# Kernel tuning notes

Measured on AMD Instinct MI355X. Metric: run time of the kernel, lower is better.

The kernel has to match this reference:

```python
import jax, jax.numpy as jnp
import numpy as np

EMBED_DIM = 1024
NUM_HEADS = 16
HEAD_DIM = EMBED_DIM // NUM_HEADS
B, T = 4, 2048


def setup_inputs() -> dict:
    key = jax.random.key(0)
    ks = jax.random.split(key, 5)
    s = 0.02
    return {
        "x": jax.random.normal(ks[0], (B, T, EMBED_DIM), dtype=jnp.float32),
        "qkv_w": jax.random.normal(ks[1], (3 * EMBED_DIM, EMBED_DIM), dtype=jnp.float32) * s,
        "qkv_b": jax.random.normal(ks[2], (3 * EMBED_DIM,), dtype=jnp.float32) * s,
        "out_w": jax.random.normal(ks[3], (EMBED_DIM, EMBED_DIM), dtype=jnp.float32) * s,
        "out_b": jax.random.normal(ks[4], (EMBED_DIM,), dtype=jnp.float32) * s,
    }


def reference(x, qkv_w, qkv_b, out_w, out_b):
    b, t, c = x.shape
    h, d = NUM_HEADS, HEAD_DIM
    # qkv projection: Linear uses y = x @ W^T + b
    qkv = jnp.einsum("btc,fc->btf", x, qkv_w) + qkv_b  # [B,T,3C]
    q, k, v = jnp.split(qkv, 3, axis=-1)
    # [B, H, T, D]
    q = q.reshape(b, t, h, d).transpose(0, 2, 1, 3)
    k = k.reshape(b, t, h, d).transpose(0, 2, 1, 3)
    v = v.reshape(b, t, h, d).transpose(0, 2, 1, 3)
    scores = jnp.einsum("bhqd,bhkd->bhqk", q, k) / jnp.sqrt(jnp.float32(d))
    causal = jnp.tril(jnp.ones((t, t), dtype=bool))
    scores = jnp.where(causal, scores, -jnp.inf)
    attn = jax.nn.softmax(scores, axis=-1)
    o = jnp.einsum("bhqk,bhkd->bhqd", attn, v)
    o = o.transpose(0, 2, 1, 3).reshape(b, t, c)
    return jnp.einsum("btc,fc->btf", o, out_w) + out_b
```

## Files before the change

### kernel.cpp

```cpp
#include <hip/hip_runtime.h>
#include <hip/hip_bf16.h>
#include <math.h>

#define SEQ   2048
#define NTOK  8192
#define EMB   1024
#define QKVF  3072

typedef __bf16 bf16;
typedef __bf16 bf16x8 __attribute__((ext_vector_type(8)));
typedef __bf16 bf16x4 __attribute__((ext_vector_type(4)));
typedef float  f32x4  __attribute__((ext_vector_type(4)));

__device__ __forceinline__ void gload_lds16(const bf16* g, bf16* l) {
    __builtin_amdgcn_global_load_lds(
        (const __attribute__((address_space(1))) unsigned int*)g,
        (__attribute__((address_space(3))) unsigned int*)l,
        16, 0, 0);
}

__global__ __launch_bounds__(256) void cvt_f32_bf16(const float* __restrict__ in,
                                                    bf16* __restrict__ out, int n) {
    int i = (blockIdx.x * 256 + threadIdx.x) * 4;
    if (i >= n) return;
    float4 f = *reinterpret_cast<const float4*>(in + i);
    bf16x4 o;
    o[0] = (bf16)f.x; o[1] = (bf16)f.y; o[2] = (bf16)f.z; o[3] = (bf16)f.w;
    *reinterpret_cast<bf16x4*>(out + i) = o;
}

template <int NF, bool BF16OUT>
__global__ __launch_bounds__(512, 2) void gemm_bt8(const bf16* __restrict__ A,
                                                   const bf16* __restrict__ Bm,
                                                   const float* __restrict__ bias,
                                                   void* __restrict__ out,
                                                   int M, int N, int K) {
    constexpr int NBR = NF / 2;
    constexpr int WN  = NBR + 2;
    __shared__ bf16 As[2][256 * 64];
    __shared__ bf16 Bs[2][2][NF * 64 * 32];

    const int nbx = N / (NF * 64);
    const int nwg = nbx * (M >> 8);
    const int q8  = nwg >> 3;
    const int swz = ((int)blockIdx.x & 7) * q8 + ((int)blockIdx.x >> 3);
    const int bx  = swz % nbx;
    const int by  = swz / nbx;

    const int tid  = threadIdx.x;
    const int lane = tid & 63;
    const int wid  = tid >> 6;
    const int wr   = wid >> 2, wc = wid & 3;
    const int lr   = lane & 15, hi = lane >> 4;
    const size_t brow = (size_t)by * 256;
    const size_t bcol = (size_t)bx * (NF * 64);

    const f32x4 fzero = {0.f, 0.f, 0.f, 0.f};
    f32x4 acc[8][NF];
#pragma unroll
    for (int m = 0; m < 8; ++m)
#pragma unroll
        for (int n = 0; n < NF; ++n) acc[m][n] = fzero;

#define STAGE_A_ROUND(b, kt, r) do {                                            \
    const int row_ = (r) * 64 + (tid >> 3);                                     \
    const int cg_  = (tid & 7) ^ (row_ & 7);                                    \
    gload_lds16(A + (brow + row_) * (size_t)K + (size_t)(kt) * 64 + cg_ * 8,    \
                &As[b][(r) * 4096 + tid * 8]);                                  \
} while (0)
#define STAGE_B_ROUND(b, kt, kkp, rr) do {                                      \
    const int row_ = (rr) * 128 + (tid >> 2);                                   \
    const int cg_  = (tid & 3) ^ (row_ & 3);                                    \
    gload_lds16(Bm + (bcol + row_) * (size_t)K + (size_t)(kt) * 64 +            \
                    (kkp) * 32 + cg_ * 8,                                       \
                &Bs[b][kkp][(rr) * 4096 + tid * 8]);                            \
} while (0)
#define ISSUE_G1(b, kt) do { STAGE_A_ROUND(b, kt, 0); STAGE_A_ROUND(b, kt, 2);  \
    for (int rr_ = 0; rr_ < NBR; ++rr_) STAGE_B_ROUND(b, kt, 0, rr_); } while (0)
#define ISSUE_G2(b, kt) do {                                                    \
    for (int rr_ = 0; rr_ < NBR; ++rr_) STAGE_B_ROUND(b, kt, 1, rr_); } while (0)
#define ISSUE_G3(b, kt) do { STAGE_A_ROUND(b, kt, 1); STAGE_A_ROUND(b, kt, 3); } while (0)

#define READ_A(b, mh, kk, dst) do {                                             \
    _Pragma("unroll")                                                           \
    for (int i_ = 0; i_ < 4; ++i_) {                                            \
        const int row_ = wr * 128 + (mh) * 64 + i_ * 16 + lr;                   \
        dst[i_] = *reinterpret_cast<const bf16x8*>(                             \
            (const char*)&As[b][0] + row_ * 128 +                               \
            (((kk) * 64 + hi * 16) ^ ((row_ & 7) << 4)));                       \
    }                                                                           \
} while (0)
#define READ_B(b, kk, dst) do {                                                 \
    _Pragma("unroll")                                                           \
    for (int n_ = 0; n_ < NF; ++n_) {                                           \
        const int row_ = wc * (NF * 16) + n_ * 16 + lr;                         \
        dst[n_] = *reinterpret_cast<const bf16x8*>(                             \
            (const char*)&Bs[b][kk][0] + row_ * 64 +                            \
            ((hi * 16) ^ ((row_ & 3) << 4)));                                   \
    }                                                                           \
} while (0)
#define DO_MFMA(mh, afr, bfr) do {                                              \
    __builtin_amdgcn_s_setprio(1);                                              \
    _Pragma("unroll")                                                           \
    for (int i_ = 0; i_ < 4; ++i_)                                              \
        _Pragma("unroll")                                                       \
        for (int n_ = 0; n_ < NF; ++n_)                                         \
            acc[(mh) * 4 + i_][n_] = __builtin_amdgcn_mfma_f32_16x16x32_bf16(   \
                afr[i_], bfr[n_], acc[(mh) * 4 + i_][n_], 0, 0, 0);             \
    __builtin_amdgcn_s_setprio(0);                                              \
} while (0)

    const int NT = K >> 6;

    ISSUE_G1(0, 0);
    ISSUE_G2(0, 0);
    ISSUE_G3(0, 0);
    asm volatile("s_waitcnt vmcnt(%0)" :: "i"(WN) : "memory");
    __builtin_amdgcn_s_barrier();

    bf16x8 af[4], bk0[NF], bk1[NF];

    for (int kt = 0; kt < NT; ++kt) {
        const int  b    = kt & 1;
        const int  nb   = b ^ 1;
        const bool last = (kt == NT - 1);

        if (!last) ISSUE_G1(nb, kt + 1);
        READ_A(b, 0, 0, af);
        READ_B(b, 0, bk0);
        if (last) asm volatile("s_waitcnt vmcnt(0)" ::: "memory");
        else      asm volatile("s_waitcnt vmcnt(%0)" :: "i"(WN) : "memory");
        __builtin_amdgcn_s_barrier();
        DO_MFMA(0, af, bk0);
        __builtin_amdgcn_s_barrier();

        if (!last) ISSUE_G2(nb, kt + 1);
        READ_A(b, 0, 1, af);
        READ_B(b, 1, bk1);
        __builtin_amdgcn_s_barrier();
        DO_MFMA(0, af, bk1);
        __builtin_amdgcn_s_barrier();

        if (!last) ISSUE_G3(nb, kt + 1);
        READ_A(b, 1, 1, af);
        __builtin_amdgcn_s_barrier();
        DO_MFMA(1, af, bk1);
        __builtin_amdgcn_s_barrier();

        READ_A(b, 1, 0, af);
        if (!last) asm volatile("s_waitcnt vmcnt(%0)" :: "i"(WN) : "memory");
        __builtin_amdgcn_s_barrier();
        DO_MFMA(1, af, bk0);
        __builtin_amdgcn_s_barrier();
    }

#pragma unroll
    for (int mf = 0; mf < 8; ++mf)
#pragma unroll
        for (int n = 0; n < NF; ++n)
#pragma unroll
            for (int r = 0; r < 4; ++r) {
                const size_t row = brow + wr * 128 + mf * 16 + hi * 4 + r;
                const size_t col = bcol + wc * (NF * 16) + n * 16 + lr;
                const float v = acc[mf][n][r] + bias[col];
                if (BF16OUT)
                    ((bf16*)out)[row * (size_t)N + col] = (bf16)v;
                else
                    ((float*)out)[row * (size_t)N + col] = v;
            }
#undef STAGE_A_ROUND
#undef STAGE_B_ROUND
#undef ISSUE_G1
#undef ISSUE_G2
#undef ISSUE_G3
#undef READ_A
#undef READ_B
#undef DO_MFMA
}

__global__ __launch_bounds__(256) void attn_kernel(const bf16* __restrict__ qkv,
                                                   bf16* __restrict__ o) {
    const int bid = blockIdx.x;
    const int qt  = 15 - (bid >> 6);
    const int bh  = bid & 63;
    const int h   = bh & 15;
    const int b   = bh >> 4;
    const int qbase = qt * 128;

    const int tid  = threadIdx.x;
    const int wv   = tid >> 6;
    const int lane = tid & 63;
    const int lr   = lane & 15, hi = lane >> 4;

    __shared__ bf16 Ks[64 * 64];
    __shared__ bf16 Vt[64 * 64];
    __shared__ bf16 Pl[4 * 32 * 64];

    char* Ksb = (char*)Ks;
    char* Vtb = (char*)Vt;
    char* Pb  = (char*)(Pl + wv * 2048);

    const size_t tokbase = (size_t)b * SEQ;

    bf16x8 aq[2][2];
#pragma unroll
    for (int qf = 0; qf < 2; ++qf) {
        const bf16* qg = qkv + (tokbase + qbase + wv * 32 + qf * 16 + lr) * (size_t)QKVF
                         + h * 64;
#pragma unroll
        for (int kk = 0; kk < 2; ++kk)
            aq[qf][kk] = *reinterpret_cast<const bf16x8*>(qg + kk * 32 + hi * 8);
    }

    const f32x4 fzero = {0.f, 0.f, 0.f, 0.f};
    f32x4 oacc[2][4];
#pragma unroll
    for (int qf = 0; qf < 2; ++qf)
#pragma unroll
        for (int n = 0; n < 4; ++n) oacc[qf][n] = fzero;
    float m_r[2] = {-__builtin_inff(), -__builtin_inff()};
    float l_r[2] = {0.f, 0.f};

    const int nkv = qt * 2 + 2;
    const float SC = 0.125f * 1.44269504f;

    const int vk0 = tid >> 3;
    const int vc  = tid & 7;

    for (int kt = 0; kt < nkv; ++kt) {
        const size_t kvrow = tokbase + (size_t)kt * 64;
        __syncthreads();

#pragma unroll
        for (int j = 0; j < 2; ++j) {
            const int kr = wv * 16 + j * 8 + (lane >> 3);
            const int cg = (lane & 7) ^ ((lane >> 3) & 7);
            gload_lds16(qkv + (kvrow + kr) * (size_t)QKVF + EMB + h * 64 + cg * 8,
                        &Ks[(wv * 16 + j * 8) * 64 + lane * 8]);
        }

        {
            bf16x8 v0 = *reinterpret_cast<const bf16x8*>(
                qkv + (kvrow + vk0) * (size_t)QKVF + 2 * EMB + h * 64 + vc * 8);
            bf16x8 v1 = *reinterpret_cast<const bf16x8*>(
                qkv + (kvrow + vk0 + 32) * (size_t)QKVF + 2 * EMB + h * 64 + vc * 8);
#pragma unroll
            for (int jj = 0; jj < 8; ++jj) {
                const int d = vc * 8 + jj;
                char* row = Vtb + d * 128;
                *(bf16*)(row + ((vk0 * 2) ^ (vc << 4)))        = v0[jj];
                *(bf16*)(row + (((vk0 + 32) * 2) ^ (vc << 4))) = v1[jj];
            }
        }
        __syncthreads();

        f32x4 s[2][4];
#pragma unroll
        for (int qf = 0; qf < 2; ++qf)
#pragma unroll
            for (int ktile = 0; ktile < 4; ++ktile) s[qf][ktile] = fzero;
#pragma unroll
        for (int ktile = 0; ktile < 4; ++ktile)
#pragma unroll
            for (int kk = 0; kk < 2; ++kk) {
                const int kr = ktile * 16 + lr;
                bf16x8 ak = *reinterpret_cast<const bf16x8*>(
                    Ksb + kr * 128 + ((kk * 64 + hi * 16) ^ ((kr & 7) << 4)));
#pragma unroll
                for (int qf = 0; qf < 2; ++qf)
                    s[qf][ktile] = __builtin_amdgcn_mfma_f32_16x16x32_bf16(
                        ak, aq[qf][kk], s[qf][ktile], 0, 0, 0);
            }

#pragma unroll
        for (int qf = 0; qf < 2; ++qf) {
            const int qglob = qbase + wv * 32 + qf * 16 + lr;
#pragma unroll
            for (int ktile = 0; ktile < 4; ++ktile) {
                const int kg0 = kt * 64 + ktile * 16 + hi * 4;
#pragma unroll
                for (int r = 0; r < 4; ++r) {
                    const float sv = s[qf][ktile][r] * SC;
                    s[qf][ktile][r] = (kg0 + r <= qglob) ? sv : -__builtin_inff();
                }
            }
        }

#pragma unroll
        for (int qf = 0; qf < 2; ++qf) {
            float tm = s[qf][0][0];
#pragma unroll
            for (int ktile = 0; ktile < 4; ++ktile)
#pragma unroll
                for (int r = 0; r < 4; ++r) tm = fmaxf(tm, s[qf][ktile][r]);
            tm = fmaxf(tm, __shfl_xor(tm, 16));
            tm = fmaxf(tm, __shfl_xor(tm, 32));

            const float mn = fmaxf(m_r[qf], tm);
            const float sc = __builtin_amdgcn_exp2f(m_r[qf] - mn);
            m_r[qf] = mn;

            float ts = 0.f;
#pragma unroll
            for (int ktile = 0; ktile < 4; ++ktile)
#pragma unroll
                for (int r = 0; r < 4; ++r) {
                    const float p = __builtin_amdgcn_exp2f(s[qf][ktile][r] - mn);
                    s[qf][ktile][r] = p;
                    ts += p;
                }
            ts += __shfl_xor(ts, 16);
            ts += __shfl_xor(ts, 32);
            l_r[qf] = l_r[qf] * sc + ts;

            float scb[4];
#pragma unroll
            for (int r = 0; r < 4; ++r) scb[r] = __shfl(sc, hi * 4 + r);
#pragma unroll
            for (int n = 0; n < 4; ++n)
#pragma unroll
                for (int r = 0; r < 4; ++r) oacc[qf][n][r] *= scb[r];

            const int q = qf * 16 + lr;
#pragma unroll
            for (int ktile = 0; ktile < 4; ++ktile) {
                bf16x4 p4;
#pragma unroll
                for (int r = 0; r < 4; ++r) p4[r] = (bf16)s[qf][ktile][r];
                *(bf16x4*)(Pb + q * 128 + ((ktile * 32 + hi * 8) ^ ((q & 7) << 4))) = p4;
            }
        }

#pragma unroll
        for (int kk = 0; kk < 2; ++kk) {
            bf16x8 ap[2];
#pragma unroll
            for (int qf = 0; qf < 2; ++qf) {
                const int q = qf * 16 + lr;
                ap[qf] = *reinterpret_cast<const bf16x8*>(
                    Pb + q * 128 + ((kk * 64 + hi * 16) ^ ((q & 7) << 4)));
            }
#pragma unroll
            for (int n = 0; n < 4; ++n) {
                const int d = n * 16 + lr;
                bf16x8 bv = *reinterpret_cast<const bf16x8*>(
                    Vtb + d * 128 + ((kk * 64 + hi * 16) ^ (((d >> 3) & 7) << 4)));
#pragma unroll
                for (int qf = 0; qf < 2; ++qf)
                    oacc[qf][n] = __builtin_amdgcn_mfma_f32_16x16x32_bf16(
                        ap[qf], bv, oacc[qf][n], 0, 0, 0);
            }
        }
    }

#pragma unroll
    for (int qf = 0; qf < 2; ++qf) {
        const float linv = 1.f / l_r[qf];
        float li[4];
#pragma unroll
        for (int r = 0; r < 4; ++r) li[r] = __shfl(linv, hi * 4 + r);
        bf16* og = o + (tokbase + qbase + wv * 32 + qf * 16) * (size_t)EMB + h * 64;
#pragma unroll
        for (int n = 0; n < 4; ++n)
#pragma unroll
            for (int r = 0; r < 4; ++r)
                og[(hi * 4 + r) * (size_t)EMB + n * 16 + lr] =
                    (bf16)(oacc[qf][n][r] * li[r]);
    }
}

extern "C" void kernel_launch(void* const* d_in, const int* in_sizes, int n_in,
                              void* d_out, int out_size, void* d_ws, size_t ws_size,
                              hipStream_t stream) {
    const float* x     = (const float*)d_in[0];
    const float* qkv_w = (const float*)d_in[1];
    const float* qkv_b = (const float*)d_in[2];
    const float* out_w = (const float*)d_in[3];
    const float* out_b = (const float*)d_in[4];
    float* out = (float*)d_out;

    char* ws = (char*)d_ws;
    bf16* x_bf    = (bf16*)(ws);
    bf16* qkvw_bf = (bf16*)(ws + 16777216);
    bf16* outw_bf = (bf16*)(ws + 23068672);
    bf16* qkv_bf  = (bf16*)(ws + 25165824);
    bf16* o_bf    = (bf16*)(ws + 75497472);

    cvt_f32_bf16<<<8192, 256, 0, stream>>>(x,     x_bf,    NTOK * EMB);
    cvt_f32_bf16<<<3072, 256, 0, stream>>>(qkv_w, qkvw_bf, QKVF * EMB);
    cvt_f32_bf16<<<1024, 256, 0, stream>>>(out_w, outw_bf, EMB * EMB);

    gemm_bt8<4, true><<<(QKVF / 256) * (NTOK / 256), 512, 0, stream>>>(
        x_bf, qkvw_bf, qkv_b, qkv_bf, NTOK, QKVF, EMB);

    attn_kernel<<<4 * 16 * (SEQ / 128), 256, 0, stream>>>(qkv_bf, o_bf);

    gemm_bt8<2, false><<<(EMB / 128) * (NTOK / 256), 512, 0, stream>>>(
        o_bf, outw_bf, out_b, out, NTOK, EMB, EMB);
}
```

Before: 315.2 us.

## Double-buffer K/V in attention, skip masked tiles, lazy softmax rescale, retune GEMM swizzle

```diff
diff --git a/kernel.cpp b/kernel.cpp
--- a/kernel.cpp
+++ b/kernel.cpp
@@ -70,7 +70,7 @@
 } while (0)
 #define STAGE_B_ROUND(b, kt, kkp, rr) do {                                      \
     const int row_ = (rr) * 128 + (tid >> 2);                                   \
-    const int cg_  = (tid & 3) ^ (row_ & 3);                                    \
+    const int cg_  = (tid & 3) ^ ((row_ >> 1) & 3);                             \
     gload_lds16(Bm + (bcol + row_) * (size_t)K + (size_t)(kt) * 64 +            \
                     (kkp) * 32 + cg_ * 8,                                       \
                 &Bs[b][kkp][(rr) * 4096 + tid * 8]);                            \
@@ -96,7 +96,7 @@
         const int row_ = wc * (NF * 16) + n_ * 16 + lr;                         \
         dst[n_] = *reinterpret_cast<const bf16x8*>(                             \
             (const char*)&Bs[b][kk][0] + row_ * 64 +                            \
-            ((hi * 16) ^ ((row_ & 3) << 4)));                                   \
+            ((hi * 16) ^ (((row_ >> 1) & 3) << 4)));                            \
     }                                                                           \
 } while (0)
 #define DO_MFMA(mh, afr, bfr) do {                                              \
@@ -192,13 +192,11 @@
     const int lane = tid & 63;
     const int lr   = lane & 15, hi = lane >> 4;
 
-    __shared__ bf16 Ks[64 * 64];
-    __shared__ bf16 Vt[64 * 64];
+    __shared__ bf16 Ks[2][64 * 64];
+    __shared__ bf16 Vt[2][64 * 64];
     __shared__ bf16 Pl[4 * 32 * 64];
 
-    char* Ksb = (char*)Ks;
-    char* Vtb = (char*)Vt;
-    char* Pb  = (char*)(Pl + wv * 2048);
+    char* Pb = (char*)(Pl + wv * 2048);
 
     const size_t tokbase = (size_t)b * SEQ;
 
@@ -226,39 +224,62 @@
 
     const int vk0 = tid >> 3;
     const int vc  = tid & 7;
+    const int kr8 = lane >> 3;
+    const int kc8 = (lane & 7) ^ ((lane >> 3) & 7);
+
+#define STAGE_K(dst, kvrow) do {                                                 \
+    _Pragma("unroll")                                                            \
+    for (int j_ = 0; j_ < 2; ++j_) {                                             \
+        const int kr_ = wv * 16 + j_ * 8 + kr8;                                  \
+        gload_lds16(qkv + ((kvrow) + kr_) * (size_t)QKVF + EMB + h * 64 + kc8*8, \
+                    &(dst)[(wv * 16 + j_ * 8) * 64 + lane * 8]);                 \
+    }                                                                            \
+} while (0)
+#define SCATTER_V(dstb, v0_, v1_) do {                                           \
+    _Pragma("unroll")                                                            \
+    for (int jj_ = 0; jj_ < 8; ++jj_) {                                          \
+        const int d_ = vc * 8 + jj_;                                             \
+        char* row_ = (dstb) + d_ * 128;                                          \
+        *(bf16*)(row_ + ((vk0 * 2) ^ (vc << 4)))        = v0_[jj_];              \
+        *(bf16*)(row_ + (((vk0 + 32) * 2) ^ (vc << 4))) = v1_[jj_];              \
+    }                                                                            \
+} while (0)
+
+    {
+        STAGE_K(Ks[0], tokbase);
+        bf16x8 v0 = *reinterpret_cast<const bf16x8*>(
+            qkv + (tokbase + vk0) * (size_t)QKVF + 2 * EMB + h * 64 + vc * 8);
+        bf16x8 v1 = *reinterpret_cast<const bf16x8*>(
+            qkv + (tokbase + vk0 + 32) * (size_t)QKVF + 2 * EMB + h * 64 + vc * 8);
+        SCATTER_V((char*)Vt[0], v0, v1);
+    }
 
     for (int kt = 0; kt < nkv; ++kt) {
-        const size_t kvrow = tokbase + (size_t)kt * 64;
+        const int bsel = kt & 1;
+        char* Ksb = (char*)Ks[bsel];
+        char* Vtb = (char*)Vt[bsel];
         __syncthreads();
 
-#pragma unroll
-        for (int j = 0; j < 2; ++j) {
-            const int kr = wv * 16 + j * 8 + (lane >> 3);
-            const int cg = (lane & 7) ^ ((lane >> 3) & 7);
-            gload_lds16(qkv + (kvrow + kr) * (size_t)QKVF + EMB + h * 64 + cg * 8,
-                        &Ks[(wv * 16 + j * 8) * 64 + lane * 8]);
+        const bool pf = (kt + 1 < nkv);
+        bf16x8 nv0, nv1;
+        if (pf) {
+            const size_t nrow = tokbase + (size_t)(kt + 1) * 64;
+            STAGE_K(Ks[bsel ^ 1], nrow);
+            nv0 = *reinterpret_cast<const bf16x8*>(
+                qkv + (nrow + vk0) * (size_t)QKVF + 2 * EMB + h * 64 + vc * 8);
+            nv1 = *reinterpret_cast<const bf16x8*>(
+                qkv + (nrow + vk0 + 32) * (size_t)QKVF + 2 * EMB + h * 64 + vc * 8);
         }
 
-        {
-            bf16x8 v0 = *reinterpret_cast<const bf16x8*>(
-                qkv + (kvrow + vk0) * (size_t)QKVF + 2 * EMB + h * 64 + vc * 8);
-            bf16x8 v1 = *reinterpret_cast<const bf16x8*>(
-                qkv + (kvrow + vk0 + 32) * (size_t)QKVF + 2 * EMB + h * 64 + vc * 8);
-#pragma unroll
-            for (int jj = 0; jj < 8; ++jj) {
-                const int d = vc * 8 + jj;
-                char* row = Vtb + d * 128;
-                *(bf16*)(row + ((vk0 * 2) ^ (vc << 4)))        = v0[jj];
-                *(bf16*)(row + (((vk0 + 32) * 2) ^ (vc << 4))) = v1[jj];
-            }
-        }
-        __syncthreads();
+        const bool act[2] = { kt * 64 <= qbase + wv * 32 + 15,
+                              kt * 64 <= qbase + wv * 32 + 31 };
 
         f32x4 s[2][4];
 #pragma unroll
         for (int qf = 0; qf < 2; ++qf)
 #pragma unroll
             for (int ktile = 0; ktile < 4; ++ktile) s[qf][ktile] = fzero;
+        __builtin_amdgcn_s_setprio(1);
 #pragma unroll
         for (int ktile = 0; ktile < 4; ++ktile)
 #pragma unroll
@@ -268,26 +289,38 @@
                     Ksb + kr * 128 + ((kk * 64 + hi * 16) ^ ((kr & 7) << 4)));
 #pragma unroll
                 for (int qf = 0; qf < 2; ++qf)
-                    s[qf][ktile] = __builtin_amdgcn_mfma_f32_16x16x32_bf16(
-                        ak, aq[qf][kk], s[qf][ktile], 0, 0, 0);
-            }
+                    if (act[qf])
+                        s[qf][ktile] = __builtin_amdgcn_mfma_f32_16x16x32_bf16(
+                            ak, aq[qf][kk], s[qf][ktile], 0, 0, 0);
+            }
+        __builtin_amdgcn_s_setprio(0);
 
 #pragma unroll
         for (int qf = 0; qf < 2; ++qf) {
+            if (!act[qf]) continue;
             const int qglob = qbase + wv * 32 + qf * 16 + lr;
-#pragma unroll
-            for (int ktile = 0; ktile < 4; ++ktile) {
-                const int kg0 = kt * 64 + ktile * 16 + hi * 4;
-#pragma unroll
-                for (int r = 0; r < 4; ++r) {
-                    const float sv = s[qf][ktile][r] * SC;
-                    s[qf][ktile][r] = (kg0 + r <= qglob) ? sv : -__builtin_inff();
+            const bool interior = (kt * 64 + 63 <= qbase + wv * 32 + qf * 16);
+            if (interior) {
+#pragma unroll
+                for (int ktile = 0; ktile < 4; ++ktile)
+#pragma unroll
+                    for (int r = 0; r < 4; ++r) s[qf][ktile][r] *= SC;
+            } else {
+#pragma unroll
+                for (int ktile = 0; ktile < 4; ++ktile) {
+                    const int kg0 = kt * 64 + ktile * 16 + hi * 4;
+#pragma unroll
+                    for (int r = 0; r < 4; ++r) {
+                        const float sv = s[qf][ktile][r] * SC;
+                        s[qf][ktile][r] = (kg0 + r <= qglob) ? sv : -__builtin_inff();
+                    }
                 }
             }
         }
 
 #pragma unroll
         for (int qf = 0; qf < 2; ++qf) {
+            if (!act[qf]) continue;
             float tm = s[qf][0][0];
 #pragma unroll
             for (int ktile = 0; ktile < 4; ++ktile)
@@ -296,30 +329,44 @@
             tm = fmaxf(tm, __shfl_xor(tm, 16));
             tm = fmaxf(tm, __shfl_xor(tm, 32));
 
-            const float mn = fmaxf(m_r[qf], tm);
-            const float sc = __builtin_amdgcn_exp2f(m_r[qf] - mn);
-            m_r[qf] = mn;
-
-            float ts = 0.f;
-#pragma unroll
-            for (int ktile = 0; ktile < 4; ++ktile)
-#pragma unroll
-                for (int r = 0; r < 4; ++r) {
-                    const float p = __builtin_amdgcn_exp2f(s[qf][ktile][r] - mn);
-                    s[qf][ktile][r] = p;
-                    ts += p;
-                }
-            ts += __shfl_xor(ts, 16);
-            ts += __shfl_xor(ts, 32);
-            l_r[qf] = l_r[qf] * sc + ts;
-
-            float scb[4];
-#pragma unroll
-            for (int r = 0; r < 4; ++r) scb[r] = __shfl(sc, hi * 4 + r);
-#pragma unroll
-            for (int n = 0; n < 4; ++n)
-#pragma unroll
-                for (int r = 0; r < 4; ++r) oacc[qf][n][r] *= scb[r];
+            if (__all(tm - m_r[qf] <= 11.5f)) {
+                const float mo = m_r[qf];
+                float ts = 0.f;
+#pragma unroll
+                for (int ktile = 0; ktile < 4; ++ktile)
+#pragma unroll
+                    for (int r = 0; r < 4; ++r) {
+                        const float p = __builtin_amdgcn_exp2f(s[qf][ktile][r] - mo);
+                        s[qf][ktile][r] = p;
+                        ts += p;
+                    }
+                ts += __shfl_xor(ts, 16);
+                ts += __shfl_xor(ts, 32);
+                l_r[qf] += ts;
+            } else {
+                const float mn = fmaxf(m_r[qf], tm);
+                const float sc = __builtin_amdgcn_exp2f(m_r[qf] - mn);
+                m_r[qf] = mn;
+                float ts = 0.f;
+#pragma unroll
+                for (int ktile = 0; ktile < 4; ++ktile)
+#pragma unroll
+                    for (int r = 0; r < 4; ++r) {
+                        const float p = __builtin_amdgcn_exp2f(s[qf][ktile][r] - mn);
+                        s[qf][ktile][r] = p;
+                        ts += p;
+                    }
+                ts += __shfl_xor(ts, 16);
+                ts += __shfl_xor(ts, 32);
+                l_r[qf] = l_r[qf] * sc + ts;
+                float scb[4];
+#pragma unroll
+                for (int r = 0; r < 4; ++r) scb[r] = __shfl(sc, hi * 4 + r);
+#pragma unroll
+                for (int n = 0; n < 4; ++n)
+#pragma unroll
+                    for (int r = 0; r < 4; ++r) oacc[qf][n][r] *= scb[r];
+            }
 
             const int q = qf * 16 + lr;
 #pragma unroll
@@ -331,15 +378,17 @@
             }
         }
 
+        __builtin_amdgcn_s_setprio(1);
 #pragma unroll
         for (int kk = 0; kk < 2; ++kk) {
             bf16x8 ap[2];
 #pragma unroll
-            for (int qf = 0; qf < 2; ++qf) {
-                const int q = qf * 16 + lr;
-                ap[qf] = *reinterpret_cast<const bf16x8*>(
-                    Pb + q * 128 + ((kk * 64 + hi * 16) ^ ((q & 7) << 4)));
-            }
+            for (int qf = 0; qf < 2; ++qf)
+                if (act[qf]) {
+                    const int q = qf * 16 + lr;
+                    ap[qf] = *reinterpret_cast<const bf16x8*>(
+                        Pb + q * 128 + ((kk * 64 + hi * 16) ^ ((q & 7) << 4)));
+                }
 #pragma unroll
             for (int n = 0; n < 4; ++n) {
                 const int d = n * 16 + lr;
@@ -347,10 +396,14 @@
                     Vtb + d * 128 + ((kk * 64 + hi * 16) ^ (((d >> 3) & 7) << 4)));
 #pragma unroll
                 for (int qf = 0; qf < 2; ++qf)
-                    oacc[qf][n] = __builtin_amdgcn_mfma_f32_16x16x32_bf16(
-                        ap[qf], bv, oacc[qf][n], 0, 0, 0);
+                    if (act[qf])
+                        oacc[qf][n] = __builtin_amdgcn_mfma_f32_16x16x32_bf16(
+                            ap[qf], bv, oacc[qf][n], 0, 0, 0);
             }
         }
+        __builtin_amdgcn_s_setprio(0);
+
+        if (pf) SCATTER_V((char*)Vt[bsel ^ 1], nv0, nv1);
     }
 
 #pragma unroll
@@ -367,6 +420,8 @@
                 og[(hi * 4 + r) * (size_t)EMB + n * 16 + lr] =
                     (bf16)(oacc[qf][n][r] * li[r]);
     }
+#undef STAGE_K
+#undef SCATTER_V
 }
 
 extern "C" void kernel_launch(void* const* d_in, const int* in_sizes, int n_in,
```

Result: slower. 335.2 us (+6.4%).
